# Kernel tuning notes

Measured on AMD Instinct MI355X. Metric: run time of the kernel, lower is better.

## Reference

```python
import jax, jax.numpy as jnp
import numpy as np

B, S, D, H, NH, E, K = 16, 512, 768, 3072, 12, 7, 2
DPH = D // NH  # 64
EPS = 1e-12


def setup_inputs() -> dict:
    key = jax.random.key(0)
    ks = jax.random.split(key, 12)
    p = lambda k, shape: (0.02 * jax.random.normal(k, shape, dtype=jnp.float32))
    return {
        "hidden_states": jax.random.normal(ks[0], (B, S, D), dtype=jnp.float32),
        "attention_mask": jnp.ones((B, S), dtype=jnp.int32),
        "ln1_g": jnp.ones((D,), jnp.float32), "ln1_b": jnp.zeros((D,), jnp.float32),
        "wq": p(ks[1], (D, D)), "bq": jnp.zeros((D,), jnp.float32),
        "wk": p(ks[2], (D, D)), "bk": jnp.zeros((D,), jnp.float32),
        "wv": p(ks[3], (D, D)), "bv": jnp.zeros((D,), jnp.float32),
        "wo": p(ks[4], (D, D)), "bo": jnp.zeros((D,), jnp.float32),
        "gate_w": p(ks[5], (D, E)), "gate_b": jnp.zeros((E,), jnp.float32),
        "w1": p(ks[6], (E, D, H)), "b1": jnp.zeros((E, H), jnp.float32),
        "w2": p(ks[7], (E, H, D)), "b2": jnp.zeros((E, D), jnp.float32),
        "ln2_g": jnp.ones((D,), jnp.float32), "ln2_b": jnp.zeros((D,), jnp.float32),
    }


def layer_norm(x, g, b):
    m = jnp.mean(x, axis=-1, keepdims=True)
    v = jnp.mean(jnp.square(x - m), axis=-1, keepdims=True)
    return g * (x - m) * jax.lax.rsqrt(v + EPS) + b


def reference(hidden_states, attention_mask, ln1_g, ln1_b, wq, bq, wk, bk, wv, bv,
              wo, bo, gate_w, gate_b, w1, b1, w2, b2, ln2_g, ln2_b):
    b, s, d = hidden_states.shape
    x = layer_norm(hidden_states, ln1_g, ln1_b)

    # DistilBERT MultiHeadSelfAttention (dropout = identity in eval)
    q = (x @ wq + bq).reshape(b, s, NH, DPH) / jnp.sqrt(jnp.float32(DPH))
    k = (x @ wk + bk).reshape(b, s, NH, DPH)
    v = (x @ wv + bv).reshape(b, s, NH, DPH)
    scores = jnp.einsum("bqhd,bkhd->bhqk", q, k)  # [B,NH,S,S]
    neg = jnp.finfo(scores.dtype).min
    scores = jnp.where(attention_mask[:, None, None, :] != 0, scores, neg)
    probs = jax.nn.softmax(scores, axis=-1)
    ctx = jnp.einsum("bhqk,bkhd->bqhd", probs, v).reshape(b, s, d)
    attn = ctx @ wo + bo
    attn = attn + hidden_states  # residual (attention_dropout = identity)

    x2 = layer_norm(attn, ln2_g, ln2_b)

    # MoE FFN: top-k sparse gating over E experts, dense compute of all experts
    gate_logits = x2 @ gate_w + gate_b  # [B,S,E]
    _, topk_idx = jax.lax.top_k(gate_logits, K)
    keep = jnp.sum(jax.nn.one_hot(topk_idx, E, dtype=gate_logits.dtype), axis=-2)  # [B,S,E]
    masked = jnp.where(keep > 0, gate_logits, jnp.finfo(gate_logits.dtype).min)
    gate_weights = jax.nn.softmax(masked, axis=-1)  # zeros outside top-k

    mid = jax.nn.gelu(jnp.einsum("bsd,edh->bseh", x2, w1) + b1, approximate=False)
    expert_out = jnp.einsum("bseh,ehd->bsed", mid, w2) + b2  # [B,S,E,D]
    ffn = jnp.einsum("bsed,bse->bsd", expert_out, gate_weights)

    out = ffn + attn  # output_dropout = identity
    return out, gate_weights
```

## Files before the change

kernel.cpp:

```cpp
#include <hip/hip_runtime.h>
#include <hip/hip_bf16.h>
#include <math.h>

#define TB 16
#define TS 512
#define TD 768
#define TH 3072
#define TNH 12
#define TE 7
#define TT (TB*TS)

typedef __bf16 bf16x8_t __attribute__((ext_vector_type(8)));
typedef __bf16 bf16x4_t __attribute__((ext_vector_type(4)));
typedef float f32x4_t __attribute__((ext_vector_type(4)));

#define NEGINF (-__builtin_huge_valf())

#define O_APL   0ULL
#define O_VT0   0ULL
#define O_VT1   12582912ULL
#define O_CTXH  37748736ULL
#define O_CTXM  50331648ULL
#define O_QKH   62914560ULL
#define O_QKM   88080384ULL
#define O_VCOL  113246208ULL
#define O_BT    138412032ULL
#define O_META  149028864ULL
#define O_MIDG  150077440ULL
#define O_X2    62914560ULL
#define O_XG    75497472ULL
#define O_W1T   0ULL
#define O_W2T   33030144ULL
#define M_CNT   0
#define M_FILL  64
#define M_NRB   192
#define M_RB2E  256
#define M_TOKE  1024
#define M_TOKW  66560
#define M_RGW   201216
#define M_TSLOT 270336

#define NRB_MAX 135
#define ROWCAP  17280

__device__ __forceinline__ void async16(const void* g, void* l) {
  __builtin_amdgcn_global_load_lds(
      (const __attribute__((address_space(1))) void*)g,
      (__attribute__((address_space(3))) void*)l, 16, 0, 0);
}

__device__ __forceinline__ void split2(float x, __bf16& h, __bf16& m) {
  h = (__bf16)x;
  m = (__bf16)(x - (float)h);
}

__device__ __forceinline__ void xcd_swizzle(int& bx, int& by, int gx, int gy) {
  int nwg = gx * gy;
  int wid = bx + by * gx;
  int q = nwg >> 3, r = nwg & 7;
  int xcd = wid & 7, pos = wid >> 3;
  int work = (xcd < r) ? xcd * (q + 1) + pos
                       : r * (q + 1) + (xcd - r) * q + pos;
  bx = work % gx;
  by = work / gx;
}

__device__ __forceinline__ float block_sum256(float v, float* red4) {
  #pragma unroll
  for (int o = 32; o > 0; o >>= 1) v += __shfl_down(v, o, 64);
  int lane = threadIdx.x & 63, wv = threadIdx.x >> 6;
  if (lane == 0) red4[wv] = v;
  __syncthreads();
  float r = red4[0] + red4[1] + red4[2] + red4[3];
  __syncthreads();
  return r;
}

__global__ void init_meta_k(int* cnt) {
  if (threadIdx.x < TE) cnt[threadIdx.x] = 0;
}

__global__ __launch_bounds__(256) void ln1_split_k(const float* __restrict__ in,
                                                   const float* __restrict__ g,
                                                   const float* __restrict__ bb,
                                                   __bf16* __restrict__ P) {
  __shared__ float red4[4];
  const size_t SA = (size_t)TT * TD;
  int row = blockIdx.x, tid = threadIdx.x;
  const float* x = in + (size_t)row * TD;
  float v0 = x[tid], v1 = x[tid + 256], v2 = x[tid + 512];
  float sum = block_sum256(v0 + v1 + v2, red4);
  float mean = sum * (1.0f / 768.0f);
  float d0 = v0 - mean, d1 = v1 - mean, d2 = v2 - mean;
  float var = block_sum256(d0*d0 + d1*d1 + d2*d2, red4) * (1.0f / 768.0f);
  float rs = rsqrtf(var + 1e-12f);
  float xn[3] = { g[tid]       * (d0 * rs) + bb[tid],
                  g[tid + 256] * (d1 * rs) + bb[tid + 256],
                  g[tid + 512] * (d2 * rs) + bb[tid + 512] };
  #pragma unroll
  for (int i = 0; i < 3; ++i) {
    __bf16 h, m; split2(xn[i], h, m);
    size_t o = (size_t)row * TD + tid + 256 * i;
    P[o] = h; P[SA + o] = m;
  }
}

__global__ void tpose_split2_k(const float* __restrict__ W0, const float* __restrict__ W1,
                               const float* __restrict__ W2,
                               __bf16* __restrict__ BT, size_t SB, int roffmul) {
  __shared__ float tile[32][33];
  const float* W = (blockIdx.z == 0) ? W0 : (blockIdx.z == 1) ? W1 : W2;
  int roff = roffmul * (int)blockIdx.z * TD;
  int c0 = blockIdx.x * 32, r0 = blockIdx.y * 32;
  int tx = threadIdx.x, ty = threadIdx.y;
  #pragma unroll
  for (int i = 0; i < 32; i += 8)
    tile[ty + i][tx] = W[(size_t)(r0 + ty + i) * TD + c0 + tx];
  __syncthreads();
  #pragma unroll
  for (int i = 0; i < 32; i += 8) {
    float x = tile[tx][ty + i];
    __bf16 h, m; split2(x, h, m);
    size_t o = (size_t)(roff + c0 + ty + i) * TD + r0 + tx;
    BT[o] = h; BT[SB + o] = m;
  }
}

template<int EPI>
__global__ __launch_bounds__(256) void gemm_split4_k(
    const __bf16* __restrict__ A0, const __bf16* __restrict__ A1,
    const __bf16* __restrict__ Bpl, size_t SB,
    const float* __restrict__ bi0, const float* __restrict__ bi1, const float* __restrict__ bi2,
    const float* __restrict__ resid, float* __restrict__ C,
    __bf16* __restrict__ qh_out, __bf16* __restrict__ qm_out, float* __restrict__ vout)
{
  __shared__ __align__(16) __bf16 As[2][4096];
  __shared__ __align__(16) __bf16 Bs[2][4096];
  const __bf16* Ap[2] = {A0, A1};
  int bx = blockIdx.x, by = blockIdx.y;
  xcd_swizzle(bx, by, gridDim.x, gridDim.y);
  int n0 = bx * 128, m0 = by * 128;
  int tid = threadIdx.x;
  int wave = tid >> 6, lane = tid & 63;
  int wr = wave >> 1, wc = wave & 1;
  int lm = lane & 15, q = lane >> 4;
  int qs = (q ^ ((lm >> 1) & 3)) * 8;
  f32x4_t acc[4][4];
  #pragma unroll
  for (int i = 0; i < 4; ++i)
    #pragma unroll
    for (int j = 0; j < 4; ++j) { f32x4_t z = {0.f,0.f,0.f,0.f}; acc[i][j] = z; }
  for (int k0 = 0; k0 < TD; k0 += 32) {
    #pragma unroll
    for (int it = 0; it < 2; ++it) {
      int f = it * 256 + tid; int r = f >> 2;
      int c8 = ((f & 3) ^ ((f >> 3) & 3)) * 8;
      #pragma unroll
      for (int p = 0; p < 2; ++p) {
        async16(Ap[p] + (size_t)(m0 + r) * TD + k0 + c8, &As[p][f * 8]);
        async16(Bpl + p * SB + (size_t)(n0 + r) * TD + k0 + c8, &Bs[p][f * 8]);
      }
    }
    __syncthreads();
    bf16x8_t af[2][4];
    #pragma unroll
    for (int pa = 0; pa < 2; ++pa)
      #pragma unroll
      for (int i = 0; i < 4; ++i)
        af[pa][i] = *(const bf16x8_t*)(&As[pa][(wr*64 + i*16 + lm) * 32 + qs]);
    #pragma unroll
    for (int pb = 0; pb < 2; ++pb) {
      bf16x8_t bfr[4];
      #pragma unroll
      for (int j = 0; j < 4; ++j)
        bfr[j] = *(const bf16x8_t*)(&Bs[pb][(wc*64 + j*16 + lm) * 32 + qs]);
      #pragma unroll
      for (int pa = 0; pa < 2 - pb; ++pa)
        #pragma unroll
        for (int i = 0; i < 4; ++i)
          #pragma unroll
          for (int j = 0; j < 4; ++j)
            acc[i][j] = __builtin_amdgcn_mfma_f32_16x16x32_bf16(af[pa][i], bfr[j], acc[i][j], 0, 0, 0);
    }
    __syncthreads();
  }
  #pragma unroll
  for (int i = 0; i < 4; ++i) {
    #pragma unroll
    for (int j = 0; j < 4; ++j) {
      #pragma unroll
      for (int r = 0; r < 4; ++r) {
        int row = m0 + wr*64 + i*16 + q*4 + r;
        int col = n0 + wc*64 + j*16 + lm;
        float v = acc[i][j][r];
        if (EPI == 0) {
          float bias = (col < 768) ? bi0[col] : (col < 1536) ? bi1[col - 768] : bi2[col - 1536];
          v += bias;
          if (col < 768) v *= 0.125f;
          if (col < 1536) {
            __bf16 hh = (__bf16)v; float r1 = v - (float)hh;
            qh_out[(size_t)row * 1536 + col] = hh;
            qm_out[(size_t)row * 1536 + col] = (__bf16)r1;
          } else {
            vout[(size_t)row * TD + (col - 1536)] = v;
          }
        } else {
          v += bi0[col] + resid[(size_t)row * TD + col];
          C[(size_t)row * TD + col] = v;
        }
      }
    }
  }
}

__global__ void vT_split2_k(const float* __restrict__ vcol,
                            __bf16* __restrict__ v0, __bf16* __restrict__ v1) {
  __shared__ float tile[32][33];
  int s0 = blockIdx.x * 32, d0 = blockIdx.y * 32, bh = blockIdx.z;
  int b = bh / 12, h = bh - b * 12;
  int tx = threadIdx.x, ty = threadIdx.y;
  #pragma unroll
  for (int i = 0; i < 32; i += 8)
    tile[ty + i][tx] = vcol[(size_t)(b * TS + s0 + ty + i) * TD + h * 64 + d0 + tx];
  __syncthreads();
  #pragma unroll
  for (int i = 0; i < 32; i += 8) {
    float x = tile[tx][ty + i];
    __bf16 hh, mm; split2(x, hh, mm);
    size_t o = (size_t)(bh * 64 + d0 + ty + i) * TS + s0 + tx;
    v0[o] = hh; v1[o] = mm;
  }
}

#define AST 72
__global__ __launch_bounds__(256) void attn_mfma_k(
    const __bf16* __restrict__ qkh, const __bf16* __restrict__ qkm,
    const __bf16* __restrict__ vT0, const __bf16* __restrict__ vT1,
    const int* __restrict__ mask,
    __bf16* __restrict__ ch, __bf16* __restrict__ cm)
{
  __shared__ __align__(16) __bf16 KS[2][64 * AST];
  __shared__ __align__(16) __bf16 VS[2][64 * AST];
  __shared__ __align__(16) __bf16 PS[2][64 * AST];
  __shared__ float maskadd[512];
  int qt = blockIdx.x, h = blockIdx.y, b = blockIdx.z;
  int tid = threadIdx.x, w = tid >> 6, lane = tid & 63;
  int lm = lane & 15, quad = lane >> 4;
  int t0 = b * TS, t0q = t0 + qt * 64, bh = b * TNH + h;
  for (int i = tid; i < 512; i += 256)
    maskadd[i] = (mask[t0 + i] != 0) ? 0.0f : -1e30f;
  #pragma unroll
  for (int it = 0; it < 2; ++it) {
    int f = it * 256 + tid, r = f >> 3, c8 = (f & 7) * 8;
    *(uint4*)&PS[0][r * AST + c8] = *(const uint4*)(qkh + (size_t)(t0q + r) * 1536 + h * 64 + c8);
    *(uint4*)&PS[1][r * AST + c8] = *(const uint4*)(qkm + (size_t)(t0q + r) * 1536 + h * 64 + c8);
  }
  __syncthreads();
  bf16x8_t qf[2][2];
  #pragma unroll
  for (int p = 0; p < 2; ++p)
    #pragma unroll
    for (int ks = 0; ks < 2; ++ks)
      qf[p][ks] = *(const bf16x8_t*)&PS[p][(w * 16 + lm) * AST + ks * 32 + quad * 8];
  __syncthreads();
  f32x4_t Oacc[4];
  #pragma unroll
  for (int j = 0; j < 4; ++j) { f32x4_t z = {0.f,0.f,0.f,0.f}; Oacc[j] = z; }
  float mst[4], lst[4];
  #pragma unroll
  for (int r = 0; r < 4; ++r) { mst[r] = -3.0e38f; lst[r] = 0.0f; }

  for (int kc = 0; kc < 8; ++kc) {
    #pragma unroll
    for (int it = 0; it < 2; ++it) {
      int f = it * 256 + tid, r = f >> 3, c8 = (f & 7) * 8;
      size_t ksrc = (size_t)(t0 + kc * 64 + r) * 1536 + 768 + h * 64 + c8;
      *(uint4*)&KS[0][r * AST + c8] = *(const uint4*)(qkh + ksrc);
      *(uint4*)&KS[1][r * AST + c8] = *(const uint4*)(qkm + ksrc);
      size_t vsrc = (size_t)(bh * 64 + r) * TS + kc * 64 + c8;
      *(uint4*)&VS[0][r * AST + c8] = *(const uint4*)(vT0 + vsrc);
      *(uint4*)&VS[1][r * AST + c8] = *(const uint4*)(vT1 + vsrc);
    }
    __syncthreads();
    f32x4_t sacc[4];
    #pragma unroll
    for (int j = 0; j < 4; ++j) { f32x4_t z = {0.f,0.f,0.f,0.f}; sacc[j] = z; }
    #pragma unroll
    for (int ks = 0; ks < 2; ++ks) {
      bf16x8_t kh_[4], km_[4];
      #pragma unroll
      for (int jn = 0; jn < 4; ++jn) {
        kh_[jn] = *(const bf16x8_t*)&KS[0][(jn*16 + lm) * AST + ks*32 + quad*8];
        km_[jn] = *(const bf16x8_t*)&KS[1][(jn*16 + lm) * AST + ks*32 + quad*8];
      }
      #pragma unroll
      for (int jn = 0; jn < 4; ++jn)
        sacc[jn] = __builtin_amdgcn_mfma_f32_16x16x32_bf16(qf[0][ks], kh_[jn], sacc[jn], 0,0,0);
      #pragma unroll
      for (int jn = 0; jn < 4; ++jn)
        sacc[jn] = __builtin_amdgcn_mfma_f32_16x16x32_bf16(qf[0][ks], km_[jn], sacc[jn], 0,0,0);
      #pragma unroll
      for (int jn = 0; jn < 4; ++jn)
        sacc[jn] = __builtin_amdgcn_mfma_f32_16x16x32_bf16(qf[1][ks], kh_[jn], sacc[jn], 0,0,0);
    }
    float s[4][4];
    #pragma unroll
    for (int jn = 0; jn < 4; ++jn)
      #pragma unroll
      for (int r = 0; r < 4; ++r)
        s[jn][r] = sacc[jn][r] + maskadd[kc*64 + jn*16 + lm];
    float alpha[4];
    #pragma unroll
    for (int r = 0; r < 4; ++r) {
      float rmax = fmaxf(fmaxf(s[0][r], s[1][r]), fmaxf(s[2][r], s[3][r]));
      #pragma unroll
      for (int mk = 1; mk < 16; mk <<= 1)
        rmax = fmaxf(rmax, __shfl_xor(rmax, mk, 64));
      float mnew = fmaxf(mst[r], rmax);
      alpha[r] = expf(mst[r] - mnew);
      mst[r] = mnew;
      float psum = 0.0f;
      #pragma unroll
      for (int jn = 0; jn < 4; ++jn) {
        float p = expf(s[jn][r] - mnew);
        s[jn][r] = p;
        psum += p;
      }
      #pragma unroll
      for (int mk = 1; mk < 16; mk <<= 1)
        psum += __shfl_xor(psum, mk, 64);
      lst[r] = lst[r] * alpha[r] + psum;
    }
    #pragma unroll
    for (int jn = 0; jn < 4; ++jn)
      #pragma unroll
      for (int r = 0; r < 4; ++r)
        Oacc[jn][r] *= alpha[r];
    #pragma unroll
    for (int jn = 0; jn < 4; ++jn)
      #pragma unroll
      for (int r = 0; r < 4; ++r) {
        __bf16 ph, pm; split2(s[jn][r], ph, pm);
        int pa = (w*16 + quad*4 + r) * AST + jn*16 + lm;
        PS[0][pa] = ph; PS[1][pa] = pm;
      }
    __syncthreads();
    #pragma unroll
    for (int ks = 0; ks < 2; ++ks) {
      bf16x8_t af[2];
      #pragma unroll
      for (int p = 0; p < 2; ++p)
        af[p] = *(const bf16x8_t*)&PS[p][(w*16 + lm) * AST + ks*32 + quad*8];
      bf16x8_t vf[2][4];
      #pragma unroll
      for (int p = 0; p < 2; ++p)
        #pragma unroll
        for (int jn = 0; jn < 4; ++jn)
          vf[p][jn] = *(const bf16x8_t*)&VS[p][(jn*16 + lm) * AST + ks*32 + quad*8];
      #pragma unroll
      for (int jn = 0; jn < 4; ++jn) {
        Oacc[jn] = __builtin_amdgcn_mfma_f32_16x16x32_bf16(af[0], vf[0][jn], Oacc[jn], 0,0,0);
        Oacc[jn] = __builtin_amdgcn_mfma_f32_16x16x32_bf16(af[0], vf[1][jn], Oacc[jn], 0,0,0);
        Oacc[jn] = __builtin_amdgcn_mfma_f32_16x16x32_bf16(af[1], vf[0][jn], Oacc[jn], 0,0,0);
      }
    }
    __syncthreads();
  }
  float linv[4];
  #pragma unroll
  for (int r = 0; r < 4; ++r) linv[r] = 1.0f / lst[r];
  #pragma unroll
  for (int jn = 0; jn < 4; ++jn)
    #pragma unroll
    for (int r = 0; r < 4; ++r) {
      float o = Oacc[jn][r] * linv[r];
      __bf16 hh, mm; split2(o, hh, mm);
      size_t oo = (size_t)(t0q + w*16 + quad*4 + r) * TD + h*64 + jn*16 + lm;
      ch[oo] = hh; cm[oo] = mm;
    }
}

__global__ __launch_bounds__(256) void ln2_gate_k(const float* __restrict__ attn,
                                                  const float* __restrict__ g,
                                                  const float* __restrict__ bb,
                                                  const float* __restrict__ gw,
                                                  const float* __restrict__ gb,
                                                  __bf16* __restrict__ x2,
                                                  float* __restrict__ gates,
                                                  int* __restrict__ tok_e,
                                                  float* __restrict__ tok_w) {
  __shared__ float red4[4];
  __shared__ float redc[4][7];
  int row = blockIdx.x, tid = threadIdx.x;
  const float* x = attn + (size_t)row * TD;
  float v0 = x[tid], v1 = x[tid + 256], v2 = x[tid + 512];
  float sum = block_sum256(v0 + v1 + v2, red4);
  float mean = sum * (1.0f / 768.0f);
  float d0 = v0 - mean, d1 = v1 - mean, d2 = v2 - mean;
  float var = block_sum256(d0*d0 + d1*d1 + d2*d2, red4) * (1.0f / 768.0f);
  float rs = rsqrtf(var + 1e-12f);
  float xn0 = g[tid]       * (d0 * rs) + bb[tid];
  float xn1 = g[tid + 256] * (d1 * rs) + bb[tid + 256];
  float xn2 = g[tid + 512] * (d2 * rs) + bb[tid + 512];
  __bf16* xo = x2 + (size_t)row * TD;
  xo[tid] = (__bf16)xn0; xo[tid + 256] = (__bf16)xn1; xo[tid + 512] = (__bf16)xn2;
  float p[7];
  const float* w0 = gw + (size_t)tid * 7;
  const float* w1p = gw + (size_t)(tid + 256) * 7;
  const float* w2p = gw + (size_t)(tid + 512) * 7;
  #pragma unroll
  for (int e = 0; e < 7; ++e) p[e] = xn0 * w0[e] + xn1 * w1p[e] + xn2 * w2p[e];
  #pragma unroll
  for (int e = 0; e < 7; ++e)
    #pragma unroll
    for (int o = 32; o > 0; o >>= 1) p[e] += __shfl_down(p[e], o, 64);
  int lane = tid & 63, wv = tid >> 6;
  if (lane == 0) {
    #pragma unroll
    for (int e = 0; e < 7; ++e) redc[wv][e] = p[e];
  }
  __syncthreads();
  if (tid == 0) {
    float l[7];
    #pragma unroll
    for (int e = 0; e < 7; ++e)
      l[e] = redc[0][e] + redc[1][e] + redc[2][e] + redc[3][e] + gb[e];
    int i1 = 0;
    for (int e = 1; e < 7; ++e) if (l[e] > l[i1]) i1 = e;
    int i2 = -1;
    for (int e = 0; e < 7; ++e) if (e != i1 && (i2 < 0 || l[e] > l[i2])) i2 = e;
    float m = l[i1];
    float e1 = expf(l[i1] - m), e2 = expf(l[i2] - m);
    float inv = 1.0f / (e1 + e2);
    float g1 = e1 * inv, g2 = e2 * inv;
    float* go = gates + (size_t)row * 7;
    #pragma unroll
    for (int e = 0; e < 7; ++e) go[e] = 0.0f;
    go[i1] = g1; go[i2] = g2;
    tok_e[row * 2] = i1; tok_e[row * 2 + 1] = i2;
    tok_w[row * 2] = g1; tok_w[row * 2 + 1] = g2;
  }
}

__global__ __launch_bounds__(256) void hist_k(const int* __restrict__ tok_e,
                                              int* __restrict__ cnt) {
  __shared__ int hloc[TE];
  int i = blockIdx.x * 256 + threadIdx.x;
  int e = tok_e[i];
  if (threadIdx.x < TE) hloc[threadIdx.x] = 0;
  __syncthreads();
  #pragma unroll
  for (int ee = 0; ee < TE; ++ee) {
    unsigned long long m = __ballot(e == ee);
    if ((threadIdx.x & 63) == 0 && m) atomicAdd(&hloc[ee], (int)__popcll(m));
  }
  __syncthreads();
  if (threadIdx.x < TE) atomicAdd(&cnt[threadIdx.x], hloc[threadIdx.x]);
}

__global__ void prefix_k(const int* __restrict__ cnt, int* __restrict__ fill,
                         int* __restrict__ nrb_p, int* __restrict__ rb2e) {
  __shared__ int start[TE + 1];
  if (threadIdx.x == 0) {
    int acc = 0;
    for (int e = 0; e < TE; ++e) {
      start[e] = acc;
      int nb = (cnt[e] + 127) >> 7;
      fill[e] = acc * 128;
      acc += nb;
    }
    start[TE] = acc;
    nrb_p[0] = acc;
  }
  __syncthreads();
  for (int b = threadIdx.x; b < start[TE]; b += blockDim.x) {
    int e = 0;
    while (start[e + 1] <= b) ++e;
    rb2e[b] = e;
  }
}

__global__ __launch_bounds__(256) void slot_assign_k(const int* __restrict__ tok_e,
                                                     const float* __restrict__ tok_w,
                                                     int* __restrict__ fill,
                                                     int* __restrict__ tok_slot,
                                                     float* __restrict__ row_gw) {
  __shared__ int wcnt[4][TE];
  __shared__ int wbase[4][TE];
  int i = blockIdx.x * 256 + threadIdx.x;
  int e = tok_e[i];
  int lane = threadIdx.x & 63, wv = threadIdx.x >> 6;
  unsigned long long lt = (1ULL << lane) - 1ULL;
  int myrank = 0;
  #pragma unroll
  for (int ee = 0; ee < TE; ++ee) {
    unsigned long long m = __ballot(e == ee);
    if (e == ee) myrank = (int)__popcll(m & lt);
    if (lane == 0) wcnt[wv][ee] = (int)__popcll(m);
  }
  __syncthreads();
  if (threadIdx.x < TE) {
    int ee = threadIdx.x;
    int c0 = wcnt[0][ee], c1 = wcnt[1][ee], c2 = wcnt[2][ee], c3 = wcnt[3][ee];
    int base = atomicAdd(&fill[ee], c0 + c1 + c2 + c3);
    wbase[0][ee] = base;
    wbase[1][ee] = base + c0;
    wbase[2][ee] = base + c0 + c1;
    wbase[3][ee] = base + c0 + c1 + c2;
  }
  __syncthreads();
  int slot = wbase[wv][e] + myrank;
  tok_slot[i] = slot;
  row_gw[slot] = tok_w[i];
}

__global__ __launch_bounds__(192) void copy_xg_k(const __bf16* __restrict__ x2,
                                                 const int* __restrict__ tok_slot,
                                                 __bf16* __restrict__ xg) {
  int t = blockIdx.x, tid = threadIdx.x;
  int j = tid / 96, c = tid - j * 96;
  int s = tok_slot[t * 2 + j];
  *(uint4*)(xg + (size_t)s * TD + c * 8) =
      *(const uint4*)(x2 + (size_t)t * TD + c * 8);
}

__global__ void transpose_cast_k(const float* __restrict__ in, __bf16* __restrict__ out,
                                 int R, int C) {
  __shared__ float tile[32][33];
  size_t zoff = (size_t)blockIdx.z * R * C;
  const float* ip = in + zoff;
  __bf16* op = out + zoff;
  int c0 = blockIdx.x * 32, r0 = blockIdx.y * 32;
  int tx = threadIdx.x, ty = threadIdx.y;
  #pragma unroll
  for (int i = 0; i < 32; i += 8)
    tile[ty + i][tx] = ip[(size_t)(r0 + ty + i) * C + c0 + tx];
  __syncthreads();
  #pragma unroll
  for (int i = 0; i < 32; i += 8)
    op[(size_t)(c0 + ty + i) * R + r0 + tx] = (__bf16)tile[tx][ty + i];
}

__global__ __launch_bounds__(256) void gemm1_k(
    const __bf16* __restrict__ xg, const __bf16* __restrict__ w1T,
    const float* __restrict__ b1, const int* __restrict__ rb2e,
    const int* __restrict__ nrb_p, int cb, __bf16* __restrict__ midg)
{
  int bx = blockIdx.x, by = blockIdx.y;
  xcd_swizzle(bx, by, gridDim.x, gridDim.y);
  int rb = cb + by;
  if (rb >= nrb_p[0]) return;
  int e = rb2e[rb];
  __shared__ __align__(16) __bf16 As[4096];
  __shared__ __align__(16) __bf16 Bs[4096];
  const __bf16* A = xg + (size_t)rb * 128 * TD;
  const __bf16* BT = w1T + (size_t)e * TH * TD;
  const float* be = b1 + (size_t)e * TH;
  int n0 = bx * 128;
  int tid = threadIdx.x;
  int wave = tid >> 6, lane = tid & 63;
  int wr = wave >> 1, wc = wave & 1;
  int lm = lane & 15, q = lane >> 4;
  int qs = (q ^ ((lm >> 1) & 3)) * 8;
  f32x4_t acc[4][4];
  #pragma unroll
  for (int i = 0; i < 4; ++i)
    #pragma unroll
    for (int j = 0; j < 4; ++j) { f32x4_t z = {0.f,0.f,0.f,0.f}; acc[i][j] = z; }
  for (int k0 = 0; k0 < TD; k0 += 32) {
    #pragma unroll
    for (int it = 0; it < 2; ++it) {
      int f = it * 256 + tid; int r = f >> 2;
      int c8 = ((f & 3) ^ ((f >> 3) & 3)) * 8;
      async16(A + (size_t)r * TD + k0 + c8, &As[f * 8]);
      async16(BT + (size_t)(n0 + r) * TD + k0 + c8, &Bs[f * 8]);
    }
    __syncthreads();
    bf16x8_t af[4], bfr[4];
    #pragma unroll
    for (int i = 0; i < 4; ++i) af[i]  = *(const bf16x8_t*)(&As[(wr*64 + i*16 + lm)*32 + qs]);
    #pragma unroll
    for (int j = 0; j < 4; ++j) bfr[j] = *(const bf16x8_t*)(&Bs[(wc*64 + j*16 + lm)*32 + qs]);
    #pragma unroll
    for (int i = 0; i < 4; ++i)
      #pragma unroll
      for (int j = 0; j < 4; ++j)
        acc[i][j] = __builtin_amdgcn_mfma_f32_16x16x32_bf16(af[i], bfr[j], acc[i][j], 0, 0, 0);
    __syncthreads();
  }
  #pragma unroll
  for (int i = 0; i < 4; ++i) {
    #pragma unroll
    for (int j = 0; j < 4; ++j) {
      #pragma unroll
      for (int r = 0; r < 4; ++r) {
        int row = wr*64 + i*16 + q*4 + r;
        int col = n0 + wc*64 + j*16 + lm;
        float v = acc[i][j][r] + be[col];
        v = 0.5f * v * (1.0f + erff(v * 0.70710678118654752f));
        midg[(size_t)(by * 128 + row) * TH + col] = (__bf16)v;
      }
    }
  }
}

__global__ __launch_bounds__(256) void gemm2_k(
    const __bf16* __restrict__ midg, const __bf16* __restrict__ w2T,
    const float* __restrict__ b2, const int* __restrict__ rb2e,
    const int* __restrict__ nrb_p, const float* __restrict__ row_gw,
    int cb, __bf16* __restrict__ part)
{
  int bx = blockIdx.x, by = blockIdx.y;
  xcd_swizzle(bx, by, gridDim.x, gridDim.y);
  int rb = cb + by;
  if (rb >= nrb_p[0]) return;
  int e = rb2e[rb];
  __shared__ __align__(16) __bf16 As[4096];
  __shared__ __align__(16) __bf16 Bs[4096];
  const __bf16* A = midg + (size_t)by * 128 * TH;
  const __bf16* BT = w2T + (size_t)e * TD * TH;
  const float* be = b2 + (size_t)e * TD;
  int n0 = bx * 128;
  int tid = threadIdx.x;
  int wave = tid >> 6, lane = tid & 63;
  int wr = wave >> 1, wc = wave & 1;
  int lm = lane & 15, q = lane >> 4;
  int qs = (q ^ ((lm >> 1) & 3)) * 8;
  f32x4_t acc[4][4];
  #pragma unroll
  for (int i = 0; i < 4; ++i)
    #pragma unroll
    for (int j = 0; j < 4; ++j) { f32x4_t z = {0.f,0.f,0.f,0.f}; acc[i][j] = z; }
  for (int k0 = 0; k0 < TH; k0 += 32) {
    #pragma unroll
    for (int it = 0; it < 2; ++it) {
      int f = it * 256 + tid; int r = f >> 2;
      int c8 = ((f & 3) ^ ((f >> 3) & 3)) * 8;
      async16(A + (size_t)r * TH + k0 + c8, &As[f * 8]);
      async16(BT + (size_t)(n0 + r) * TH + k0 + c8, &Bs[f * 8]);
    }
    __syncthreads();
    bf16x8_t af[4], bfr[4];
    #pragma unroll
    for (int i = 0; i < 4; ++i) af[i]  = *(const bf16x8_t*)(&As[(wr*64 + i*16 + lm)*32 + qs]);
    #pragma unroll
    for (int j = 0; j < 4; ++j) bfr[j] = *(const bf16x8_t*)(&Bs[(wc*64 + j*16 + lm)*32 + qs]);
    #pragma unroll
    for (int i = 0; i < 4; ++i)
      #pragma unroll
      for (int j = 0; j < 4; ++j)
        acc[i][j] = __builtin_amdgcn_mfma_f32_16x16x32_bf16(af[i], bfr[j], acc[i][j], 0, 0, 0);
    __syncthreads();
  }
  #pragma unroll
  for (int i = 0; i < 4; ++i) {
    #pragma unroll
    for (int r = 0; r < 4; ++r) {
      int row = wr*64 + i*16 + q*4 + r;
      int grow = rb * 128 + row;
      float gwt = row_gw[grow];
      #pragma unroll
      for (int j = 0; j < 4; ++j) {
        int col = n0 + wc*64 + j*16 + lm;
        part[(size_t)grow * TD + col] = (__bf16)(gwt * (acc[i][j][r] + be[col]));
      }
    }
  }
}

__global__ __launch_bounds__(192) void gather_k(const __bf16* __restrict__ part,
                                                const int* __restrict__ tok_slot,
                                                float* __restrict__ outp) {
  int t = blockIdx.x, tid = threadIdx.x;
  int s0 = tok_slot[t * 2], s1 = tok_slot[t * 2 + 1];
  int c = tid * 4;
  float4 o = *(float4*)(outp + (size_t)t * TD + c);
  bf16x4_t p0 = *(const bf16x4_t*)(part + (size_t)s0 * TD + c);
  bf16x4_t p1 = *(const bf16x4_t*)(part + (size_t)s1 * TD + c);
  o.x += (float)p0[0] + (float)p1[0];
  o.y += (float)p0[1] + (float)p1[1];
  o.z += (float)p0[2] + (float)p1[2];
  o.w += (float)p0[3] + (float)p1[3];
  *(float4*)(outp + (size_t)t * TD + c) = o;
}

extern "C" void kernel_launch(void* const* d_in, const int* in_sizes, int n_in,
                              void* d_out, int out_size, void* d_ws, size_t ws_size,
                              hipStream_t stream) {
  (void)in_sizes; (void)n_in; (void)out_size;
  const float* hidden = (const float*)d_in[0];
  const int*   mask   = (const int*)d_in[1];
  const float* ln1_g  = (const float*)d_in[2];
  const float* ln1_b  = (const float*)d_in[3];
  const float* wq = (const float*)d_in[4];  const float* bq = (const float*)d_in[5];
  const float* wk = (const float*)d_in[6];  const float* bk = (const float*)d_in[7];
  const float* wv = (const float*)d_in[8];  const float* bv = (const float*)d_in[9];
  const float* wo = (const float*)d_in[10]; const float* bo = (const float*)d_in[11];
  const float* gate_w = (const float*)d_in[12];
  const float* gate_b = (const float*)d_in[13];
  const float* w1 = (const float*)d_in[14];
  const float* b1 = (const float*)d_in[15];
  const float* w2 = (const float*)d_in[16];
  const float* b2 = (const float*)d_in[17];
  const float* ln2_g = (const float*)d_in[18];
  const float* ln2_b = (const float*)d_in[19];

  float* outp  = (float*)d_out;
  float* gates = (float*)d_out + (size_t)TT * TD;

  char* ws = (char*)d_ws;
  __bf16* Apl  = (__bf16*)(ws + O_APL);
  __bf16* vT0p = (__bf16*)(ws + O_VT0);
  __bf16* vT1p = (__bf16*)(ws + O_VT1);
  __bf16* ctxh = (__bf16*)(ws + O_CTXH);
  __bf16* ctxm = (__bf16*)(ws + O_CTXM);
  __bf16* qkh  = (__bf16*)(ws + O_QKH);
  __bf16* qkm  = (__bf16*)(ws + O_QKM);
  float*  vcol = (float*)(ws + O_VCOL);
  __bf16* BTp  = (__bf16*)(ws + O_BT);
  __bf16* x2   = (__bf16*)(ws + O_X2);
  __bf16* xg   = (__bf16*)(ws + O_XG);
  __bf16* w1T  = (__bf16*)(ws + O_W1T);
  __bf16* w2T  = (__bf16*)(ws + O_W2T);
  char*   meta = ws + O_META;
  int*   cnt      = (int*)(meta + M_CNT);
  int*   fill     = (int*)(meta + M_FILL);
  int*   nrb_p    = (int*)(meta + M_NRB);
  int*   rb2e     = (int*)(meta + M_RB2E);
  int*   tok_e    = (int*)(meta + M_TOKE);
  float* tok_w    = (float*)(meta + M_TOKW);
  float* row_gw   = (float*)(meta + M_RGW);
  int*   tok_slot = (int*)(meta + M_TSLOT);
  __bf16* midg = (__bf16*)(ws + O_MIDG);

  long long midcap = (long long)ws_size - (long long)O_MIDG;
  int crb = (int)(midcap / (128LL * TH * 2));
  if (crb < 1) crb = 1;
  if (crb > NRB_MAX) crb = NRB_MAX;

  const size_t SA = (size_t)TT * TD;

  init_meta_k<<<1, 64, 0, stream>>>(cnt);
  ln1_split_k<<<TT, 256, 0, stream>>>(hidden, ln1_g, ln1_b, Apl);
  tpose_split2_k<<<dim3(24, 24, 3), dim3(32, 8), 0, stream>>>(
      wq, wk, wv, BTp, (size_t)2304 * TD, 1);
  gemm_split4_k<0><<<dim3(18, 64), 256, 0, stream>>>(
      Apl, Apl + SA, BTp, (size_t)2304 * TD,
      bq, bk, bv, nullptr, nullptr, qkh, qkm, vcol);
  vT_split2_k<<<dim3(16, 2, 192), dim3(32, 8), 0, stream>>>(vcol, vT0p, vT1p);
  attn_mfma_k<<<dim3(8, TNH, TB), 256, 0, stream>>>(
      qkh, qkm, vT0p, vT1p, mask, ctxh, ctxm);
  tpose_split2_k<<<dim3(24, 24, 1), dim3(32, 8), 0, stream>>>(
      wo, wo, wo, BTp, (size_t)TD * TD, 0);
  gemm_split4_k<1><<<dim3(6, 64), 256, 0, stream>>>(
      ctxh, ctxm, BTp, (size_t)TD * TD,
      bo, nullptr, nullptr, hidden, outp, nullptr, nullptr, nullptr);
  ln2_gate_k<<<TT, 256, 0, stream>>>(outp, ln2_g, ln2_b, gate_w, gate_b, x2, gates,
                                     tok_e, tok_w);
  hist_k<<<64, 256, 0, stream>>>(tok_e, cnt);
  prefix_k<<<1, 192, 0, stream>>>(cnt, fill, nrb_p, rb2e);
  slot_assign_k<<<64, 256, 0, stream>>>(tok_e, tok_w, fill, tok_slot, row_gw);
  copy_xg_k<<<TT, 192, 0, stream>>>(x2, tok_slot, xg);
  transpose_cast_k<<<dim3(TH / 32, TD / 32, TE), dim3(32, 8), 0, stream>>>(w1, w1T, TD, TH);
  transpose_cast_k<<<dim3(TD / 32, TH / 32, TE), dim3(32, 8), 0, stream>>>(w2, w2T, TH, TD);
  __bf16* part = xg;
  for (int cb = 0; cb < NRB_MAX; cb += crb) {
    int nb = NRB_MAX - cb; if (nb > crb) nb = crb;
    gemm1_k<<<dim3(TH / 128, nb), 256, 0, stream>>>(xg, w1T, b1, rb2e, nrb_p, cb, midg);
    gemm2_k<<<dim3(TD / 128, nb), 256, 0, stream>>>(midg, w2T, b2, rb2e, nrb_p,
                                                    row_gw, cb, part);
  }
  gather_k<<<TT, 192, 0, stream>>>(part, tok_slot, outp);
}
```

Before: 815.5 us.

## Split-K expert GEMM2 with atomic scatter into output, deepen K step

The second expert GEMM is split over two K halves via a grid z dimension. Each block scatters its gate-weighted result straight into the output with float atomics, using a new row-to-token map. This removes the bf16 partial buffer and the separate gather kernel, and doubles the number of GEMM2 blocks. Both expert GEMMs now load 64 K-columns per barrier, halving synchronisations at the cost of doubled LDS. Float atomics make the summation order nondeterministic and add atomic traffic, and padded rows are skipped through a new -1 init kernel.

```diff
diff --git a/kernel.cpp b/kernel.cpp
--- a/kernel.cpp
+++ b/kernel.cpp
@@ -39,6 +39,7 @@
 #define M_TOKW  66560
 #define M_RGW   201216
 #define M_TSLOT 270336
+#define M_RTOK  335872
 
 #define NRB_MAX 135
 #define ROWCAP  17280
@@ -78,6 +79,11 @@
 
 __global__ void init_meta_k(int* cnt) {
   if (threadIdx.x < TE) cnt[threadIdx.x] = 0;
+}
+
+__global__ __launch_bounds__(256) void init_rtok_k(int* row_tok) {
+  int i = blockIdx.x * 256 + threadIdx.x;
+  if (i < ROWCAP) row_tok[i] = -1;
 }
 
 __global__ __launch_bounds__(256) void ln1_split_k(const float* __restrict__ in,
@@ -484,7 +490,8 @@
                                                      const float* __restrict__ tok_w,
                                                      int* __restrict__ fill,
                                                      int* __restrict__ tok_slot,
-                                                     float* __restrict__ row_gw) {
+                                                     float* __restrict__ row_gw,
+                                                     int* __restrict__ row_tok) {
   __shared__ int wcnt[4][TE];
   __shared__ int wbase[4][TE];
   int i = blockIdx.x * 256 + threadIdx.x;
@@ -512,6 +519,7 @@
   int slot = wbase[wv][e] + myrank;
   tok_slot[i] = slot;
   row_gw[slot] = tok_w[i];
+  row_tok[slot] = i >> 1;
 }
 
 __global__ __launch_bounds__(192) void copy_xg_k(const __bf16* __restrict__ x2,
@@ -551,8 +559,8 @@
   int rb = cb + by;
   if (rb >= nrb_p[0]) return;
   int e = rb2e[rb];
-  __shared__ __align__(16) __bf16 As[4096];
-  __shared__ __align__(16) __bf16 Bs[4096];
+  __shared__ __align__(16) __bf16 As[2][4096];
+  __shared__ __align__(16) __bf16 Bs[2][4096];
   const __bf16* A = xg + (size_t)rb * 128 * TD;
   const __bf16* BT = w1T + (size_t)e * TH * TD;
   const float* be = b1 + (size_t)e * TH;
@@ -567,25 +575,30 @@
   for (int i = 0; i < 4; ++i)
     #pragma unroll
     for (int j = 0; j < 4; ++j) { f32x4_t z = {0.f,0.f,0.f,0.f}; acc[i][j] = z; }
-  for (int k0 = 0; k0 < TD; k0 += 32) {
+  for (int k0 = 0; k0 < TD; k0 += 64) {
     #pragma unroll
     for (int it = 0; it < 2; ++it) {
       int f = it * 256 + tid; int r = f >> 2;
       int c8 = ((f & 3) ^ ((f >> 3) & 3)) * 8;
-      async16(A + (size_t)r * TD + k0 + c8, &As[f * 8]);
-      async16(BT + (size_t)(n0 + r) * TD + k0 + c8, &Bs[f * 8]);
-    }
-    __syncthreads();
-    bf16x8_t af[4], bfr[4];
-    #pragma unroll
-    for (int i = 0; i < 4; ++i) af[i]  = *(const bf16x8_t*)(&As[(wr*64 + i*16 + lm)*32 + qs]);
-    #pragma unroll
-    for (int j = 0; j < 4; ++j) bfr[j] = *(const bf16x8_t*)(&Bs[(wc*64 + j*16 + lm)*32 + qs]);
-    #pragma unroll
-    for (int i = 0; i < 4; ++i)
-      #pragma unroll
-      for (int j = 0; j < 4; ++j)
-        acc[i][j] = __builtin_amdgcn_mfma_f32_16x16x32_bf16(af[i], bfr[j], acc[i][j], 0, 0, 0);
+      async16(A + (size_t)r * TD + k0 + c8, &As[0][f * 8]);
+      async16(A + (size_t)r * TD + k0 + 32 + c8, &As[1][f * 8]);
+      async16(BT + (size_t)(n0 + r) * TD + k0 + c8, &Bs[0][f * 8]);
+      async16(BT + (size_t)(n0 + r) * TD + k0 + 32 + c8, &Bs[1][f * 8]);
+    }
+    __syncthreads();
+    #pragma unroll
+    for (int ks = 0; ks < 2; ++ks) {
+      bf16x8_t af[4], bfr[4];
+      #pragma unroll
+      for (int i = 0; i < 4; ++i) af[i]  = *(const bf16x8_t*)(&As[ks][(wr*64 + i*16 + lm)*32 + qs]);
+      #pragma unroll
+      for (int j = 0; j < 4; ++j) bfr[j] = *(const bf16x8_t*)(&Bs[ks][(wc*64 + j*16 + lm)*32 + qs]);
+      #pragma unroll
+      for (int i = 0; i < 4; ++i)
+        #pragma unroll
+        for (int j = 0; j < 4; ++j)
+          acc[i][j] = __builtin_amdgcn_mfma_f32_16x16x32_bf16(af[i], bfr[j], acc[i][j], 0, 0, 0);
+    }
     __syncthreads();
   }
   #pragma unroll
@@ -608,17 +621,18 @@
     const __bf16* __restrict__ midg, const __bf16* __restrict__ w2T,
     const float* __restrict__ b2, const int* __restrict__ rb2e,
     const int* __restrict__ nrb_p, const float* __restrict__ row_gw,
-    int cb, __bf16* __restrict__ part)
+    const int* __restrict__ row_tok, int cb, float* __restrict__ outp)
 {
   int bx = blockIdx.x, by = blockIdx.y;
   xcd_swizzle(bx, by, gridDim.x, gridDim.y);
   int rb = cb + by;
   if (rb >= nrb_p[0]) return;
   int e = rb2e[rb];
-  __shared__ __align__(16) __bf16 As[4096];
-  __shared__ __align__(16) __bf16 Bs[4096];
-  const __bf16* A = midg + (size_t)by * 128 * TH;
-  const __bf16* BT = w2T + (size_t)e * TD * TH;
+  int kz = blockIdx.z;
+  __shared__ __align__(16) __bf16 As[2][4096];
+  __shared__ __align__(16) __bf16 Bs[2][4096];
+  const __bf16* A = midg + (size_t)by * 128 * TH + kz * 1536;
+  const __bf16* BT = w2T + (size_t)e * TD * TH + kz * 1536;
   const float* be = b2 + (size_t)e * TD;
   int n0 = bx * 128;
   int tid = threadIdx.x;
@@ -631,25 +645,30 @@
   for (int i = 0; i < 4; ++i)
     #pragma unroll
     for (int j = 0; j < 4; ++j) { f32x4_t z = {0.f,0.f,0.f,0.f}; acc[i][j] = z; }
-  for (int k0 = 0; k0 < TH; k0 += 32) {
+  for (int k0 = 0; k0 < 1536; k0 += 64) {
     #pragma unroll
     for (int it = 0; it < 2; ++it) {
       int f = it * 256 + tid; int r = f >> 2;
       int c8 = ((f & 3) ^ ((f >> 3) & 3)) * 8;
-      async16(A + (size_t)r * TH + k0 + c8, &As[f * 8]);
-      async16(BT + (size_t)(n0 + r) * TH + k0 + c8, &Bs[f * 8]);
-    }
-    __syncthreads();
-    bf16x8_t af[4], bfr[4];
-    #pragma unroll
-    for (int i = 0; i < 4; ++i) af[i]  = *(const bf16x8_t*)(&As[(wr*64 + i*16 + lm)*32 + qs]);
-    #pragma unroll
-    for (int j = 0; j < 4; ++j) bfr[j] = *(const bf16x8_t*)(&Bs[(wc*64 + j*16 + lm)*32 + qs]);
-    #pragma unroll
-    for (int i = 0; i < 4; ++i)
-      #pragma unroll
-      for (int j = 0; j < 4; ++j)
-        acc[i][j] = __builtin_amdgcn_mfma_f32_16x16x32_bf16(af[i], bfr[j], acc[i][j], 0, 0, 0);
+      async16(A + (size_t)r * TH + k0 + c8, &As[0][f * 8]);
+      async16(A + (size_t)r * TH + k0 + 32 + c8, &As[1][f * 8]);
+      async16(BT + (size_t)(n0 + r) * TH + k0 + c8, &Bs[0][f * 8]);
+      async16(BT + (size_t)(n0 + r) * TH + k0 + 32 + c8, &Bs[1][f * 8]);
+    }
+    __syncthreads();
+    #pragma unroll
+    for (int ks = 0; ks < 2; ++ks) {
+      bf16x8_t af[4], bfr[4];
+      #pragma unroll
+      for (int i = 0; i < 4; ++i) af[i]  = *(const bf16x8_t*)(&As[ks][(wr*64 + i*16 + lm)*32 + qs]);
+      #pragma unroll
+      for (int j = 0; j < 4; ++j) bfr[j] = *(const bf16x8_t*)(&Bs[ks][(wc*64 + j*16 + lm)*32 + qs]);
+      #pragma unroll
+      for (int i = 0; i < 4; ++i)
+        #pragma unroll
+        for (int j = 0; j < 4; ++j)
+          acc[i][j] = __builtin_amdgcn_mfma_f32_16x16x32_bf16(af[i], bfr[j], acc[i][j], 0, 0, 0);
+    }
     __syncthreads();
   }
   #pragma unroll
@@ -658,30 +677,18 @@
     for (int r = 0; r < 4; ++r) {
       int row = wr*64 + i*16 + q*4 + r;
       int grow = rb * 128 + row;
-      float gwt = row_gw[grow];
-      #pragma unroll
-      for (int j = 0; j < 4; ++j) {
-        int col = n0 + wc*64 + j*16 + lm;
-        part[(size_t)grow * TD + col] = (__bf16)(gwt * (acc[i][j][r] + be[col]));
+      int tok = row_tok[grow];
+      if (tok >= 0) {
+        float gwt = row_gw[grow];
+        #pragma unroll
+        for (int j = 0; j < 4; ++j) {
+          int col = n0 + wc*64 + j*16 + lm;
+          float v = acc[i][j][r] + ((kz == 0) ? be[col] : 0.0f);
+          atomicAdd(&outp[(size_t)tok * TD + col], gwt * v);
+        }
       }
     }
   }
-}
-
-__global__ __launch_bounds__(192) void gather_k(const __bf16* __restrict__ part,
-                                                const int* __restrict__ tok_slot,
-                                                float* __restrict__ outp) {
-  int t = blockIdx.x, tid = threadIdx.x;
-  int s0 = tok_slot[t * 2], s1 = tok_slot[t * 2 + 1];
-  int c = tid * 4;
-  float4 o = *(float4*)(outp + (size_t)t * TD + c);
-  bf16x4_t p0 = *(const bf16x4_t*)(part + (size_t)s0 * TD + c);
-  bf16x4_t p1 = *(const bf16x4_t*)(part + (size_t)s1 * TD + c);
-  o.x += (float)p0[0] + (float)p1[0];
-  o.y += (float)p0[1] + (float)p1[1];
-  o.z += (float)p0[2] + (float)p1[2];
-  o.w += (float)p0[3] + (float)p1[3];
-  *(float4*)(outp + (size_t)t * TD + c) = o;
 }
 
 extern "C" void kernel_launch(void* const* d_in, const int* in_sizes, int n_in,
@@ -731,6 +738,7 @@
   float* tok_w    = (float*)(meta + M_TOKW);
   float* row_gw   = (float*)(meta + M_RGW);
   int*   tok_slot = (int*)(meta + M_TSLOT);
+  int*   row_tok  = (int*)(meta + M_RTOK);
   __bf16* midg = (__bf16*)(ws + O_MIDG);
 
   long long midcap = (long long)ws_size - (long long)O_MIDG;
@@ -741,6 +749,7 @@
   const size_t SA = (size_t)TT * TD;
 
   init_meta_k<<<1, 64, 0, stream>>>(cnt);
+  init_rtok_k<<<(ROWCAP + 255) / 256, 256, 0, stream>>>(row_tok);
   ln1_split_k<<<TT, 256, 0, stream>>>(hidden, ln1_g, ln1_b, Apl);
   tpose_split2_k<<<dim3(24, 24, 3), dim3(32, 8), 0, stream>>>(
       wq, wk, wv, BTp, (size_t)2304 * TD, 1);
@@ -759,16 +768,14 @@
                                      tok_e, tok_w);
   hist_k<<<64, 256, 0, stream>>>(tok_e, cnt);
   prefix_k<<<1, 192, 0, stream>>>(cnt, fill, nrb_p, rb2e);
-  slot_assign_k<<<64, 256, 0, stream>>>(tok_e, tok_w, fill, tok_slot, row_gw);
+  slot_assign_k<<<64, 256, 0, stream>>>(tok_e, tok_w, fill, tok_slot, row_gw, row_tok);
   copy_xg_k<<<TT, 192, 0, stream>>>(x2, tok_slot, xg);
   transpose_cast_k<<<dim3(TH / 32, TD / 32, TE), dim3(32, 8), 0, stream>>>(w1, w1T, TD, TH);
   transpose_cast_k<<<dim3(TD / 32, TH / 32, TE), dim3(32, 8), 0, stream>>>(w2, w2T, TH, TD);
-  __bf16* part = xg;
   for (int cb = 0; cb < NRB_MAX; cb += crb) {
     int nb = NRB_MAX - cb; if (nb > crb) nb = crb;
     gemm1_k<<<dim3(TH / 128, nb), 256, 0, stream>>>(xg, w1T, b1, rb2e, nrb_p, cb, midg);
-    gemm2_k<<<dim3(TD / 128, nb), 256, 0, stream>>>(midg, w2T, b2, rb2e, nrb_p,
-                                                    row_gw, cb, part);
-  }
-  gather_k<<<TT, 192, 0, stream>>>(part, tok_slot, outp);
-}
+    gemm2_k<<<dim3(TD / 128, nb, 2), 256, 0, stream>>>(midg, w2T, b2, rb2e, nrb_p,
+                                                       row_gw, row_tok, cb, outp);
+  }
+}
```

After: 896.6 us. +10.0%, slower.
